# Optimization experiments

Hardware: AMD Instinct MI355X
Metric: run time of the kernel (lower is better)

## Reference

```python
import jax, jax.numpy as jnp
import numpy as np

N_NODES = 50000
N_EDGES = 1200000
IN_CH = 128
HID = 64
HEADS = 1
OUT_CH = 64
NEG_SLOPE = 0.2


def setup_inputs() -> dict:
    key = jax.random.key(0)
    ks = jax.random.split(key, 9)
    x = jax.random.normal(ks[0], (N_NODES, IN_CH), dtype=jnp.float32)
    edge_index = jax.random.randint(ks[1], (2, N_EDGES), 0, N_NODES, dtype=jnp.int64)
    edge_weight = jax.random.uniform(ks[2], (N_EDGES,), dtype=jnp.float32)
    # GATv2Conv params: separate lin_l / lin_r (share_weights=False), attention vector, bias
    s_in = 1.0 / np.sqrt(IN_CH)
    W_l = jax.random.uniform(ks[3], (HEADS * HID, IN_CH), minval=-s_in, maxval=s_in, dtype=jnp.float32)
    W_r = jax.random.uniform(ks[4], (HEADS * HID, IN_CH), minval=-s_in, maxval=s_in, dtype=jnp.float32)
    att = jax.random.normal(ks[5], (HEADS, HID), dtype=jnp.float32) * (1.0 / np.sqrt(HID))
    bias_conv = jnp.zeros((HEADS * HID,), dtype=jnp.float32)
    s_h = 1.0 / np.sqrt(HEADS * HID)
    W_lin = jax.random.uniform(ks[6], (OUT_CH, HEADS * HID), minval=-s_h, maxval=s_h, dtype=jnp.float32)
    b_lin = jax.random.uniform(ks[7], (OUT_CH,), minval=-s_h, maxval=s_h, dtype=jnp.float32)
    return {"x": x, "edge_index": edge_index, "edge_weight": edge_weight,
            "W_l": W_l, "W_r": W_r, "att": att, "bias_conv": bias_conv,
            "W_lin": W_lin, "b_lin": b_lin}


def reference(x, edge_index, edge_weight, W_l, W_r, att, bias_conv, W_lin, b_lin):
    N = x.shape[0]
    H, C = att.shape
    # add self loops (GATv2Conv default add_self_loops=True)
    loop = jnp.arange(N, dtype=edge_index.dtype)
    src = jnp.concatenate([edge_index[0], loop])  # [E+N] source j
    dst = jnp.concatenate([edge_index[1], loop])  # [E+N] target i
    # linear projections -> [N, H, C]
    xl = (x @ W_l.T).reshape(N, H, C)
    xr = (x @ W_r.T).reshape(N, H, C)
    # per-edge GATv2 logits: att . LeakyReLU(xl_j + xr_i)
    e = jax.nn.leaky_relu(xl[src] + xr[dst], NEG_SLOPE)       # [E, H, C]
    logits = jnp.einsum('ehc,hc->eh', e, att)                 # [E, H]
    # segment softmax over incoming edges of each target node
    m = jax.ops.segment_max(logits, dst, num_segments=N)       # [N, H]
    m = jnp.where(jnp.isfinite(m), m, 0.0)
    expv = jnp.exp(logits - m[dst])                            # [E, H]
    denom = jax.ops.segment_sum(expv, dst, num_segments=N)     # [N, H]
    alpha = expv / (denom[dst] + 1e-16)                        # [E, H]
    # dropout(p=0.2) on alpha: identity in eval mode
    # scatter-weighted aggregation of source features
    msg = alpha[:, :, None] * xl[src]                          # [E, H, C]
    out = jax.ops.segment_sum(msg, dst, num_segments=N)        # [N, H, C]
    out = out.reshape(N, H * C) + bias_conv
    out = jax.nn.elu(out)
    return out @ W_lin.T + b_lin
```

## Files before the change

kernel.cpp:

```cpp
#include <hip/hip_runtime.h>

#define IN_CH 128
#define HID 64
#define NEG 0.2f

typedef short bf16x8 __attribute__((ext_vector_type(8)));
typedef float f32x4  __attribute__((ext_vector_type(4)));

__device__ __forceinline__ unsigned short f2bf(float f) {
    unsigned u = __float_as_uint(f);
    u += 0x7fffu + ((u >> 16) & 1u);
    return (unsigned short)(u >> 16);
}
__device__ __forceinline__ float bf2f(unsigned short h) {
    return __uint_as_float((unsigned)h << 16);
}

__global__ __launch_bounds__(512, 4) void proj_part(
    const float* __restrict__ x, const float* __restrict__ W_l,
    const float* __restrict__ W_r,
    unsigned short* __restrict__ xlb, float* __restrict__ xr,
    const int* __restrict__ src, const int* __restrict__ dst,
    int* __restrict__ gcursor, unsigned* __restrict__ pairs,
    int nN, int E)
{
    __shared__ unsigned short A_hi[64 * 136];
    __shared__ unsigned short A_lo[64 * 136];
    int tid = threadIdx.x;
    int nb = blockIdx.x * 64;
    int lane = tid & 63;
    int wid = __builtin_amdgcn_readfirstlane(tid >> 6);
    int mat = wid >> 2;
    int ct  = (wid & 3) * 16;
    int n = lane & 15, quad = lane >> 4;

    const float* __restrict__ W = mat ? W_r : W_l;
    bf16x8 Bh[4], Bl[4];
    #pragma unroll
    for (int s = 0; s < 4; ++s) {
        const float* wr = W + (size_t)(ct + n) * IN_CH + s * 32 + quad * 8;
        float4 w0 = *(const float4*)(wr);
        float4 w1 = *(const float4*)(wr + 4);
        float wf[8] = {w0.x, w0.y, w0.z, w0.w, w1.x, w1.y, w1.z, w1.w};
        #pragma unroll
        for (int j = 0; j < 8; ++j) {
            unsigned short h = f2bf(wf[j]);
            Bh[s][j] = (short)h;
            Bl[s][j] = (short)f2bf(wf[j] - bf2f(h));
        }
    }

    #pragma unroll
    for (int it = 0; it < 2; ++it) {
        int gi = it * 512 + tid;
        int row = gi >> 4, c8 = gi & 15;
        int node = nb + row;
        uint4 hi = make_uint4(0, 0, 0, 0), lo = make_uint4(0, 0, 0, 0);
        if (node < nN) {
            const float* xp = x + (size_t)node * IN_CH + c8 * 8;
            float4 f0 = *(const float4*)(xp);
            float4 f1 = *(const float4*)(xp + 4);
            float xf[8] = {f0.x, f0.y, f0.z, f0.w, f1.x, f1.y, f1.z, f1.w};
            unsigned hh[8], ll[8];
            #pragma unroll
            for (int j = 0; j < 8; ++j) {
                unsigned short h = f2bf(xf[j]);
                hh[j] = h;
                ll[j] = f2bf(xf[j] - bf2f(h));
            }
            hi = make_uint4(hh[0] | (hh[1] << 16), hh[2] | (hh[3] << 16),
                            hh[4] | (hh[5] << 16), hh[6] | (hh[7] << 16));
            lo = make_uint4(ll[0] | (ll[1] << 16), ll[2] | (ll[3] << 16),
                            ll[4] | (ll[5] << 16), ll[6] | (ll[7] << 16));
        }
        *(uint4*)(&A_hi[row * 136 + c8 * 8]) = hi;
        *(uint4*)(&A_lo[row * 136 + c8 * 8]) = lo;
    }
    __syncthreads();

    #pragma unroll
    for (int mt = 0; mt < 4; ++mt) {
        f32x4 d = {0.f, 0.f, 0.f, 0.f};
        int arow = (mt * 16 + n) * 136 + quad * 8;
        #pragma unroll
        for (int s = 0; s < 4; ++s) {
            bf16x8 ah = *(const bf16x8*)(&A_hi[arow + s * 32]);
            bf16x8 al = *(const bf16x8*)(&A_lo[arow + s * 32]);
            d = __builtin_amdgcn_mfma_f32_16x16x32_bf16(ah, Bh[s], d, 0, 0, 0);
            d = __builtin_amdgcn_mfma_f32_16x16x32_bf16(ah, Bl[s], d, 0, 0, 0);
            d = __builtin_amdgcn_mfma_f32_16x16x32_bf16(al, Bh[s], d, 0, 0, 0);
        }
        #pragma unroll
        for (int r = 0; r < 4; ++r) {
            int node = nb + mt * 16 + quad * 4 + r;
            if (node < nN) {
                if (mat)
                    xr[(size_t)node * HID + ct + n] = d[r];
                else
                    xlb[(size_t)node * HID + ct + n] = f2bf(d[r]);
            }
        }
    }

    __syncthreads();
    int* lh = (int*)A_hi;
    int* lb = (int*)A_lo;
    for (int i = tid; i < 4096; i += 512) lh[i] = 0;
    __syncthreads();

    int G = (int)gridDim.x;
    int C = ((E + G - 1) / G + 3) & ~3;
    int lo = blockIdx.x * C;
    int hi = lo + C; if (hi > E) hi = E;

    int i0 = lo + tid * 4;
    unsigned pay[4];
    int bk[4], rk[4];
    int ne = 0;
    if (i0 + 3 < hi) {
        int4 s4 = *(const int4*)(src + i0);
        int4 d4 = *(const int4*)(dst + i0);
        bk[0] = d4.x >> 4; pay[0] = (unsigned)s4.x | (((unsigned)d4.x & 15u) << 16);
        bk[1] = d4.y >> 4; pay[1] = (unsigned)s4.y | (((unsigned)d4.y & 15u) << 16);
        bk[2] = d4.z >> 4; pay[2] = (unsigned)s4.z | (((unsigned)d4.z & 15u) << 16);
        bk[3] = d4.w >> 4; pay[3] = (unsigned)s4.w | (((unsigned)d4.w & 15u) << 16);
        ne = 4;
        #pragma unroll
        for (int q = 0; q < 4; ++q) rk[q] = atomicAdd(&lh[bk[q]], 1);
    } else {
        for (int j = i0; j < hi; ++j) {
            int s = src[j], d = dst[j];
            bk[ne] = d >> 4;
            pay[ne] = (unsigned)s | (((unsigned)d & 15u) << 16);
            rk[ne] = atomicAdd(&lh[bk[ne]], 1);
            ++ne;
        }
    }
    __syncthreads();
    for (int i = tid; i < 4096; i += 512) {
        int c = lh[i];
        lb[i] = c ? atomicAdd(&gcursor[i], c) : 0;
    }
    __syncthreads();
    for (int q = 0; q < ne; ++q) {
        int p = lb[bk[q]] + rk[q];
        if (p < 512) pairs[(bk[q] << 9) + p] = pay[q];
    }
}

__global__ __launch_bounds__(256, 8) void gat_sorted(
    const unsigned short* __restrict__ xlb, const float* __restrict__ xr,
    const unsigned* __restrict__ pairs, const int* __restrict__ bcnt,
    const float* __restrict__ att, const float* __restrict__ bias_conv,
    const float* __restrict__ W_lin, const float* __restrict__ b_lin,
    float* __restrict__ out, int nN)
{
    __shared__ unsigned short sorted[512];
    __shared__ unsigned short Hhi[16 * 72];
    __shared__ unsigned short Hlo[16 * 72];
    __shared__ int cnt[16];
    __shared__ int rs[17];
    int tid = threadIdx.x;
    if (tid < 16) cnt[tid] = 0;
    __syncthreads();

    int blk = blockIdx.x;
    int M = bcnt[blk];
    if (M > 512) M = 512;
    const unsigned* __restrict__ pb = pairs + ((size_t)blk << 9);

    unsigned ew[2];
    int dl[2], rk[2];
    int ne = 0;
    for (int i = tid; i < M; i += 256) {
        unsigned w = pb[i];
        ew[ne] = w;
        dl[ne] = (w >> 16) & 15;
        rk[ne] = atomicAdd(&cnt[dl[ne]], 1);
        ++ne;
    }
    __syncthreads();
    if (tid < 16) {
        int c = cnt[tid];
        int s = c;
        #pragma unroll
        for (int d = 1; d < 16; d <<= 1) {
            int t = __shfl_up(s, d, 64);
            if (tid >= d) s += t;
        }
        rs[tid] = s - c;
        if (tid == 15) rs[16] = s;
    }
    __syncthreads();
    for (int q = 0; q < ne; ++q)
        sorted[rs[dl[q]] + rk[q]] = (unsigned short)(ew[q] & 0xFFFFu);
    __syncthreads();

    int lane = tid & 63, wv = tid >> 6;
    int g = lane >> 4, gl = lane & 15;
    const float4 att4 = *(const float4*)(att + gl * 4);
    const float c1 = 0.5f * (1.f + NEG), c2 = 0.5f * (1.f - NEG);
    float4 a1 = make_float4(c1 * att4.x, c1 * att4.y, c1 * att4.z, c1 * att4.w);
    float4 a2 = make_float4(c2 * att4.x, c2 * att4.y, c2 * att4.z, c2 * att4.w);
    int nb = blk * 16;
    for (int t = 0; t < 4; ++t) {
        int nl = wv * 4 + t;
        int node = nb + nl;
        if (node >= nN) break;
        const float4 xr4 = *(const float4*)(xr + (size_t)node * HID + gl * 4);
        float4 acc = make_float4(0.f, 0.f, 0.f, 0.f);
        float denom = 0.f;
        if (g == 0) {
            ushort4 us = *(const ushort4*)(xlb + (size_t)node * HID + gl * 4);
            float xsx = bf2f(us.x), xsy = bf2f(us.y), xsz = bf2f(us.z), xsw = bf2f(us.w);
            float tx = xsx + xr4.x, ty = xsy + xr4.y;
            float tz = xsz + xr4.z, tw = xsw + xr4.w;
            float r = a1.x * tx;
            r = fmaf(a2.x, fabsf(tx), r);
            r = fmaf(a1.y, ty, r); r = fmaf(a2.y, fabsf(ty), r);
            r = fmaf(a1.z, tz, r); r = fmaf(a2.z, fabsf(tz), r);
            r = fmaf(a1.w, tw, r); r = fmaf(a2.w, fabsf(tw), r);
            r += __shfl_xor(r, 1, 64);
            r += __shfl_xor(r, 2, 64);
            r += __shfl_xor(r, 4, 64);
            r += __shfl_xor(r, 8, 64);
            float ev = __expf(r);
            denom = ev;
            acc.x = ev * xsx; acc.y = ev * xsy;
            acc.z = ev * xsz; acc.w = ev * xsw;
        }
        int s0 = rs[nl], s1 = rs[nl + 1];
        int last = s1 - 1;
        for (int base = s0; base < s1; base += 16) {
            int kb = base + g * 4;
            int k0 = (kb     <= last) ? kb     : last;
            int k1 = (kb + 1 <= last) ? kb + 1 : last;
            int k2 = (kb + 2 <= last) ? kb + 2 : last;
            int k3 = (kb + 3 <= last) ? kb + 3 : last;
            int j0 = sorted[k0], j1 = sorted[k1], j2 = sorted[k2], j3 = sorted[k3];
            ushort4 ua = *(const ushort4*)(xlb + (size_t)j0 * HID + gl * 4);
            ushort4 ub = *(const ushort4*)(xlb + (size_t)j1 * HID + gl * 4);
            ushort4 uc = *(const ushort4*)(xlb + (size_t)j2 * HID + gl * 4);
            ushort4 ud = *(const ushort4*)(xlb + (size_t)j3 * HID + gl * 4);
            float xax = bf2f(ua.x), xay = bf2f(ua.y), xaz = bf2f(ua.z), xaw = bf2f(ua.w);
            float xbx = bf2f(ub.x), xby = bf2f(ub.y), xbz = bf2f(ub.z), xbw = bf2f(ub.w);
            float xcx = bf2f(uc.x), xcy = bf2f(uc.y), xcz = bf2f(uc.z), xcw = bf2f(uc.w);
            float xdx = bf2f(ud.x), xdy = bf2f(ud.y), xdz = bf2f(ud.z), xdw = bf2f(ud.w);

            float t0, t1, t2, t3, ra, rb, rc, rd;
            t0 = xax + xr4.x; t1 = xay + xr4.y; t2 = xaz + xr4.z; t3 = xaw + xr4.w;
            ra = a1.x * t0;        ra = fmaf(a2.x, fabsf(t0), ra);
            ra = fmaf(a1.y, t1, ra); ra = fmaf(a2.y, fabsf(t1), ra);
            ra = fmaf(a1.z, t2, ra); ra = fmaf(a2.z, fabsf(t2), ra);
            ra = fmaf(a1.w, t3, ra); ra = fmaf(a2.w, fabsf(t3), ra);
            t0 = xbx + xr4.x; t1 = xby + xr4.y; t2 = xbz + xr4.z; t3 = xbw + xr4.w;
            rb = a1.x * t0;        rb = fmaf(a2.x, fabsf(t0), rb);
            rb = fmaf(a1.y, t1, rb); rb = fmaf(a2.y, fabsf(t1), rb);
            rb = fmaf(a1.z, t2, rb); rb = fmaf(a2.z, fabsf(t2), rb);
            rb = fmaf(a1.w, t3, rb); rb = fmaf(a2.w, fabsf(t3), rb);
            t0 = xcx + xr4.x; t1 = xcy + xr4.y; t2 = xcz + xr4.z; t3 = xcw + xr4.w;
            rc = a1.x * t0;        rc = fmaf(a2.x, fabsf(t0), rc);
            rc = fmaf(a1.y, t1, rc); rc = fmaf(a2.y, fabsf(t1), rc);
            rc = fmaf(a1.z, t2, rc); rc = fmaf(a2.z, fabsf(t2), rc);
            rc = fmaf(a1.w, t3, rc); rc = fmaf(a2.w, fabsf(t3), rc);
            t0 = xdx + xr4.x; t1 = xdy + xr4.y; t2 = xdz + xr4.z; t3 = xdw + xr4.w;
            rd = a1.x * t0;        rd = fmaf(a2.x, fabsf(t0), rd);
            rd = fmaf(a1.y, t1, rd); rd = fmaf(a2.y, fabsf(t1), rd);
            rd = fmaf(a1.z, t2, rd); rd = fmaf(a2.z, fabsf(t2), rd);
            rd = fmaf(a1.w, t3, rd); rd = fmaf(a2.w, fabsf(t3), rd);

            ra += __shfl_xor(ra, 1, 64); rb += __shfl_xor(rb, 1, 64);
            rc += __shfl_xor(rc, 1, 64); rd += __shfl_xor(rd, 1, 64);
            ra += __shfl_xor(ra, 2, 64); rb += __shfl_xor(rb, 2, 64);
            rc += __shfl_xor(rc, 2, 64); rd += __shfl_xor(rd, 2, 64);
            ra += __shfl_xor(ra, 4, 64); rb += __shfl_xor(rb, 4, 64);
            rc += __shfl_xor(rc, 4, 64); rd += __shfl_xor(rd, 4, 64);
            ra += __shfl_xor(ra, 8, 64); rb += __shfl_xor(rb, 8, 64);
            rc += __shfl_xor(rc, 8, 64); rd += __shfl_xor(rd, 8, 64);

            float ea = (kb     < s1) ? __expf(ra) : 0.f;
            float eb = (kb + 1 < s1) ? __expf(rb) : 0.f;
            float ec = (kb + 2 < s1) ? __expf(rc) : 0.f;
            float ed = (kb + 3 < s1) ? __expf(rd) : 0.f;
            denom += (ea + eb) + (ec + ed);
            acc.x = fmaf(ea, xax, acc.x); acc.x = fmaf(eb, xbx, acc.x);
            acc.x = fmaf(ec, xcx, acc.x); acc.x = fmaf(ed, xdx, acc.x);
            acc.y = fmaf(ea, xay, acc.y); acc.y = fmaf(eb, xby, acc.y);
            acc.y = fmaf(ec, xcy, acc.y); acc.y = fmaf(ed, xdy, acc.y);
            acc.z = fmaf(ea, xaz, acc.z); acc.z = fmaf(eb, xbz, acc.z);
            acc.z = fmaf(ec, xcz, acc.z); acc.z = fmaf(ed, xdz, acc.z);
            acc.w = fmaf(ea, xaw, acc.w); acc.w = fmaf(eb, xbw, acc.w);
            acc.w = fmaf(ec, xcw, acc.w); acc.w = fmaf(ed, xdw, acc.w);
        }
        denom += __shfl_xor(denom, 16, 64);
        denom += __shfl_xor(denom, 32, 64);
        acc.x += __shfl_xor(acc.x, 16, 64); acc.x += __shfl_xor(acc.x, 32, 64);
        acc.y += __shfl_xor(acc.y, 16, 64); acc.y += __shfl_xor(acc.y, 32, 64);
        acc.z += __shfl_xor(acc.z, 16, 64); acc.z += __shfl_xor(acc.z, 32, 64);
        acc.w += __shfl_xor(acc.w, 16, 64); acc.w += __shfl_xor(acc.w, 32, 64);
        float inv = 1.f / (denom + 1e-16f);
        float4 b4 = *(const float4*)(bias_conv + gl * 4);
        float hx = fmaf(acc.x, inv, b4.x);
        float hy = fmaf(acc.y, inv, b4.y);
        float hz = fmaf(acc.z, inv, b4.z);
        float hw = fmaf(acc.w, inv, b4.w);
        hx = (hx > 0.f) ? hx : (__expf(hx) - 1.f);
        hy = (hy > 0.f) ? hy : (__expf(hy) - 1.f);
        hz = (hz > 0.f) ? hz : (__expf(hz) - 1.f);
        hw = (hw > 0.f) ? hw : (__expf(hw) - 1.f);
        if (g == 0) {
            unsigned short hix = f2bf(hx), hiy = f2bf(hy),
                           hiz = f2bf(hz), hiw = f2bf(hw);
            ushort4 vhi = make_ushort4(hix, hiy, hiz, hiw);
            ushort4 vlo = make_ushort4(f2bf(hx - bf2f(hix)), f2bf(hy - bf2f(hiy)),
                                       f2bf(hz - bf2f(hiz)), f2bf(hw - bf2f(hiw)));
            *(ushort4*)(&Hhi[nl * 72 + gl * 4]) = vhi;
            *(ushort4*)(&Hlo[nl * 72 + gl * 4]) = vlo;
        }
    }
    __syncthreads();

    bf16x8 Wh[2], Wl[2];
    #pragma unroll
    for (int s = 0; s < 2; ++s) {
        const float* wr = W_lin + (size_t)(wv * 16 + gl) * HID + s * 32 + g * 8;
        float4 w0 = *(const float4*)(wr);
        float4 w1 = *(const float4*)(wr + 4);
        float wf[8] = {w0.x, w0.y, w0.z, w0.w, w1.x, w1.y, w1.z, w1.w};
        #pragma unroll
        for (int j = 0; j < 8; ++j) {
            unsigned short h = f2bf(wf[j]);
            Wh[s][j] = (short)h;
            Wl[s][j] = (short)f2bf(wf[j] - bf2f(h));
        }
    }
    float blin = b_lin[wv * 16 + gl];
    {
        f32x4 d = {0.f, 0.f, 0.f, 0.f};
        int arow = gl * 72 + g * 8;
        #pragma unroll
        for (int s = 0; s < 2; ++s) {
            bf16x8 ah = *(const bf16x8*)(&Hhi[arow + s * 32]);
            bf16x8 al = *(const bf16x8*)(&Hlo[arow + s * 32]);
            d = __builtin_amdgcn_mfma_f32_16x16x32_bf16(ah, Wh[s], d, 0, 0, 0);
            d = __builtin_amdgcn_mfma_f32_16x16x32_bf16(ah, Wl[s], d, 0, 0, 0);
            d = __builtin_amdgcn_mfma_f32_16x16x32_bf16(al, Wh[s], d, 0, 0, 0);
        }
        #pragma unroll
        for (int r = 0; r < 4; ++r) {
            int node = nb + g * 4 + r;
            if (node < nN)
                out[(size_t)node * HID + wv * 16 + gl] = d[r] + blin;
        }
    }
}

extern "C" void kernel_launch(void* const* d_in, const int* in_sizes, int n_in,
                              void* d_out, int out_size, void* d_ws, size_t ws_size,
                              hipStream_t stream) {
    const float* x      = (const float*)d_in[0];
    const int*   ei     = (const int*)d_in[1];
    const float* W_l    = (const float*)d_in[3];
    const float* W_r    = (const float*)d_in[4];
    const float* att    = (const float*)d_in[5];
    const float* bias_c = (const float*)d_in[6];
    const float* W_lin  = (const float*)d_in[7];
    const float* b_lin  = (const float*)d_in[8];
    float* out = (float*)d_out;

    int N = in_sizes[0] / IN_CH;
    int E = in_sizes[2];
    const int* srcp = ei;
    const int* dstp = ei + E;
    int NB = (N + 63) / 64;
    int NQ = (N + 15) / 16;

    char* ws = (char*)d_ws;
    float* xr = (float*)ws;
    unsigned short* xlb = (unsigned short*)(xr + (size_t)N * HID);
    int* gcursor = (int*)(xlb + (size_t)N * HID);
    unsigned* pairs = (unsigned*)(gcursor + 4096);

    hipMemsetAsync(gcursor, 0, 4096 * sizeof(int), stream);
    proj_part<<<NB, 512, 0, stream>>>(x, W_l, W_r, xlb, xr, srcp, dstp,
                                      gcursor, pairs, N, E);
    gat_sorted<<<NQ, 256, 0, stream>>>(xlb, xr, pairs, gcursor,
                                       att, bias_c, W_lin, b_lin, out, N);
}
```

Measured before the change: 176.3 us.

## Coarsen edge partition buckets to 64 nodes and split into quarters in gather

```diff
diff --git a/kernel.cpp b/kernel.cpp
--- a/kernel.cpp
+++ b/kernel.cpp
@@ -104,8 +104,8 @@
 
     __syncthreads();
     int* lh = (int*)A_hi;
-    int* lb = (int*)A_lo;
-    for (int i = tid; i < 4096; i += 512) lh[i] = 0;
+    int* lb = lh + 1024;
+    for (int i = tid; i < 1024; i += 512) lh[i] = 0;
     __syncthreads();
 
     int G = (int)gridDim.x;
@@ -120,31 +120,31 @@
     if (i0 + 3 < hi) {
         int4 s4 = *(const int4*)(src + i0);
         int4 d4 = *(const int4*)(dst + i0);
-        bk[0] = d4.x >> 4; pay[0] = (unsigned)s4.x | (((unsigned)d4.x & 15u) << 16);
-        bk[1] = d4.y >> 4; pay[1] = (unsigned)s4.y | (((unsigned)d4.y & 15u) << 16);
-        bk[2] = d4.z >> 4; pay[2] = (unsigned)s4.z | (((unsigned)d4.z & 15u) << 16);
-        bk[3] = d4.w >> 4; pay[3] = (unsigned)s4.w | (((unsigned)d4.w & 15u) << 16);
+        bk[0] = d4.x >> 6; pay[0] = (unsigned)s4.x | (((unsigned)d4.x & 63u) << 16);
+        bk[1] = d4.y >> 6; pay[1] = (unsigned)s4.y | (((unsigned)d4.y & 63u) << 16);
+        bk[2] = d4.z >> 6; pay[2] = (unsigned)s4.z | (((unsigned)d4.z & 63u) << 16);
+        bk[3] = d4.w >> 6; pay[3] = (unsigned)s4.w | (((unsigned)d4.w & 63u) << 16);
         ne = 4;
         #pragma unroll
         for (int q = 0; q < 4; ++q) rk[q] = atomicAdd(&lh[bk[q]], 1);
     } else {
         for (int j = i0; j < hi; ++j) {
             int s = src[j], d = dst[j];
-            bk[ne] = d >> 4;
-            pay[ne] = (unsigned)s | (((unsigned)d & 15u) << 16);
+            bk[ne] = d >> 6;
+            pay[ne] = (unsigned)s | (((unsigned)d & 63u) << 16);
             rk[ne] = atomicAdd(&lh[bk[ne]], 1);
             ++ne;
         }
     }
     __syncthreads();
-    for (int i = tid; i < 4096; i += 512) {
+    for (int i = tid; i < 1024; i += 512) {
         int c = lh[i];
         lb[i] = c ? atomicAdd(&gcursor[i], c) : 0;
     }
     __syncthreads();
     for (int q = 0; q < ne; ++q) {
         int p = lb[bk[q]] + rk[q];
-        if (p < 512) pairs[(bk[q] << 9) + p] = pay[q];
+        if (p < 2048) pairs[(bk[q] << 11) + p] = pay[q];
     }
 }
 
@@ -165,19 +165,24 @@
     __syncthreads();
 
     int blk = blockIdx.x;
-    int M = bcnt[blk];
-    if (M > 512) M = 512;
-    const unsigned* __restrict__ pb = pairs + ((size_t)blk << 9);
-
-    unsigned ew[2];
-    int dl[2], rk[2];
+    int b  = blk >> 2;
+    int qq = blk & 3;
+    int M = bcnt[b];
+    if (M > 2048) M = 2048;
+    const unsigned* __restrict__ pb = pairs + ((size_t)b << 11);
+
+    unsigned ew[8];
+    int ml[8];
     int ne = 0;
     for (int i = tid; i < M; i += 256) {
         unsigned w = pb[i];
-        ew[ne] = w;
-        dl[ne] = (w >> 16) & 15;
-        rk[ne] = atomicAdd(&cnt[dl[ne]], 1);
-        ++ne;
+        if (((w >> 20) & 3u) == (unsigned)qq) {
+            int dl = (w >> 16) & 15;
+            int r = atomicAdd(&cnt[dl], 1);
+            ew[ne] = w;
+            ml[ne] = (r << 4) | dl;
+            ++ne;
+        }
     }
     __syncthreads();
     if (tid < 16) {
@@ -188,12 +193,16 @@
             int t = __shfl_up(s, d, 64);
             if (tid >= d) s += t;
         }
-        rs[tid] = s - c;
-        if (tid == 15) rs[16] = s;
-    }
-    __syncthreads();
-    for (int q = 0; q < ne; ++q)
-        sorted[rs[dl[q]] + rk[q]] = (unsigned short)(ew[q] & 0xFFFFu);
+        int st = s - c;
+        rs[tid] = st > 512 ? 512 : st;
+        if (tid == 15) rs[16] = s > 512 ? 512 : s;
+    }
+    __syncthreads();
+    for (int q = 0; q < ne; ++q) {
+        int dl = ml[q] & 15;
+        int p = rs[dl] + (ml[q] >> 4);
+        if (p < 512) sorted[p] = (unsigned short)(ew[q] & 0xFFFFu);
+    }
     __syncthreads();
 
     int lane = tid & 63, wv = tid >> 6;
@@ -202,7 +211,7 @@
     const float c1 = 0.5f * (1.f + NEG), c2 = 0.5f * (1.f - NEG);
     float4 a1 = make_float4(c1 * att4.x, c1 * att4.y, c1 * att4.z, c1 * att4.w);
     float4 a2 = make_float4(c2 * att4.x, c2 * att4.y, c2 * att4.z, c2 * att4.w);
-    int nb = blk * 16;
+    int nb = b * 64 + qq * 16;
     for (int t = 0; t < 4; ++t) {
         int nl = wv * 4 + t;
         int node = nb + nl;
@@ -373,17 +382,16 @@
     const int* srcp = ei;
     const int* dstp = ei + E;
     int NB = (N + 63) / 64;
-    int NQ = (N + 15) / 16;
 
     char* ws = (char*)d_ws;
     float* xr = (float*)ws;
     unsigned short* xlb = (unsigned short*)(xr + (size_t)N * HID);
     int* gcursor = (int*)(xlb + (size_t)N * HID);
-    unsigned* pairs = (unsigned*)(gcursor + 4096);
-
-    hipMemsetAsync(gcursor, 0, 4096 * sizeof(int), stream);
+    unsigned* pairs = (unsigned*)(gcursor + 1024);
+
+    hipMemsetAsync(gcursor, 0, 1024 * sizeof(int), stream);
     proj_part<<<NB, 512, 0, stream>>>(x, W_l, W_r, xlb, xr, srcp, dstp,
                                       gcursor, pairs, N, E);
-    gat_sorted<<<NQ, 256, 0, stream>>>(xlb, xr, pairs, gcursor,
-                                       att, bias_c, W_lin, b_lin, out, N);
-}
+    gat_sorted<<<NB * 4, 256, 0, stream>>>(xlb, xr, pairs, gcursor,
+                                           att, bias_c, W_lin, b_lin, out, N);
+}
```

After: 173.9 us. No clear change (-1.4%).

## Concentrate edge bucketing into a quarter of the projection blocks

Applied to the files above, without the earlier changes.

```diff
diff --git a/kernel.cpp b/kernel.cpp
--- a/kernel.cpp
+++ b/kernel.cpp
@@ -103,48 +103,65 @@
     }
 
     __syncthreads();
-    int* lh = (int*)A_hi;
-    int* lb = (int*)A_lo;
-    for (int i = tid; i < 4096; i += 512) lh[i] = 0;
-    __syncthreads();
-
-    int G = (int)gridDim.x;
-    int C = ((E + G - 1) / G + 3) & ~3;
-    int lo = blockIdx.x * C;
-    int hi = lo + C; if (hi > E) hi = E;
-
-    int i0 = lo + tid * 4;
-    unsigned pay[4];
-    int bk[4], rk[4];
-    int ne = 0;
-    if (i0 + 3 < hi) {
-        int4 s4 = *(const int4*)(src + i0);
-        int4 d4 = *(const int4*)(dst + i0);
-        bk[0] = d4.x >> 4; pay[0] = (unsigned)s4.x | (((unsigned)d4.x & 15u) << 16);
-        bk[1] = d4.y >> 4; pay[1] = (unsigned)s4.y | (((unsigned)d4.y & 15u) << 16);
-        bk[2] = d4.z >> 4; pay[2] = (unsigned)s4.z | (((unsigned)d4.z & 15u) << 16);
-        bk[3] = d4.w >> 4; pay[3] = (unsigned)s4.w | (((unsigned)d4.w & 15u) << 16);
-        ne = 4;
-        #pragma unroll
-        for (int q = 0; q < 4; ++q) rk[q] = atomicAdd(&lh[bk[q]], 1);
-    } else {
-        for (int j = i0; j < hi; ++j) {
-            int s = src[j], d = dst[j];
-            bk[ne] = d >> 4;
-            pay[ne] = (unsigned)s | (((unsigned)d & 15u) << 16);
-            rk[ne] = atomicAdd(&lh[bk[ne]], 1);
-            ++ne;
-        }
-    }
-    __syncthreads();
-    for (int i = tid; i < 4096; i += 512) {
-        int c = lh[i];
-        lb[i] = c ? atomicAdd(&gcursor[i], c) : 0;
-    }
-    __syncthreads();
-    for (int q = 0; q < ne; ++q) {
-        int p = lb[bk[q]] + rk[q];
-        if (p < 512) pairs[(bk[q] << 9) + p] = pay[q];
+    int PB = ((int)gridDim.x + 3) >> 2;
+    if ((int)blockIdx.x < PB) {
+        int* lh = (int*)A_hi;
+        int* lb = (int*)A_lo;
+        for (int i = tid; i < 4096; i += 512) lh[i] = 0;
+        __syncthreads();
+
+        int C = ((E + PB - 1) / PB + 3) & ~3;
+        int lo = blockIdx.x * C;
+        int hi = lo + C; if (hi > E) hi = E;
+
+        unsigned pw[12];
+        unsigned rk[12];
+        #pragma unroll
+        for (int s = 0; s < 3; ++s) {
+            int i0 = lo + s * 2048 + tid * 4;
+            int4 s4, d4;
+            bool full = (i0 + 3 < hi);
+            if (full) {
+                s4 = *(const int4*)(src + i0);
+                d4 = *(const int4*)(dst + i0);
+            }
+            #pragma unroll
+            for (int j = 0; j < 4; ++j) {
+                int q = s * 4 + j;
+                int e = i0 + j;
+                int sv = 0, dv = 0;
+                bool ok;
+                if (full) {
+                    sv = (&s4.x)[j]; dv = (&d4.x)[j]; ok = true;
+                } else {
+                    ok = (e < hi);
+                    if (ok) { sv = src[e]; dv = dst[e]; }
+                }
+                if (ok) {
+                    int b = dv >> 4;
+                    pw[q] = (unsigned)sv | (((unsigned)dv & 15u) << 16)
+                                         | ((unsigned)b << 20);
+                    rk[q] = (unsigned)atomicAdd(&lh[b], 1);
+                } else {
+                    pw[q] = 0xFFFFFFFFu;
+                    rk[q] = 0;
+                }
+            }
+        }
+        __syncthreads();
+        for (int i = tid; i < 4096; i += 512) {
+            int c = lh[i];
+            lb[i] = c ? atomicAdd(&gcursor[i], c) : 0;
+        }
+        __syncthreads();
+        #pragma unroll
+        for (int q = 0; q < 12; ++q) {
+            if (pw[q] != 0xFFFFFFFFu) {
+                int b = (int)(pw[q] >> 20);
+                int p = lb[b] + (int)rk[q];
+                if (p < 512) pairs[(b << 9) + p] = pw[q] & 0xFFFFFu;
+            }
+        }
     }
 }
 
```

Result: faster. 164.0 us, median of 3 (-7.0%).
